# Optimization experiments

Measured on AMD Instinct MI355X. Metric: run time of the kernel, lower is better.

The kernel has to match this reference:

```python
import jax, jax.numpy as jnp
import numpy as np

DIM = 512
HEADS = 16
GRID = (32, 32)
MLP_HIDDEN = 2048
EPS = 1e-5


def _relative_position_index(hw):
    H, W = hw
    coords = np.stack(np.meshgrid(np.arange(H), np.arange(W), indexing='ij'))  # [2,H,W]
    coords = coords.reshape(2, -1)  # [2, L]
    rel = coords[:, :, None] - coords[:, None, :]  # [2, L, L]
    rel = rel.transpose(1, 2, 0).astype(np.int64)  # [L, L, 2]
    rel[:, :, 0] += H - 1
    rel[:, :, 1] += W - 1
    rel[:, :, 0] *= 2 * W - 1
    return jnp.asarray(rel.sum(-1))  # [L, L]


def setup_inputs() -> dict:
    key = jax.random.key(0)
    ks = jax.random.split(key, 12)
    L = GRID[0] * GRID[1]
    table_size = (2 * GRID[0] - 1) * (2 * GRID[1] - 1)
    s = 0.02
    return {
        'x': jax.random.normal(ks[0], (8, L, DIM), jnp.float32),
        'rel_index': _relative_position_index(GRID),
        'bias_table': s * jax.random.truncated_normal(ks[1], -2.0, 2.0, (table_size, HEADS), jnp.float32),
        'qkv_w': jax.random.normal(ks[2], (DIM, 3 * DIM), jnp.float32) / np.sqrt(DIM),
        'qkv_b': jnp.zeros((3 * DIM,), jnp.float32),
        'proj_w': jax.random.normal(ks[3], (DIM, DIM), jnp.float32) / np.sqrt(DIM),
        'proj_b': jnp.zeros((DIM,), jnp.float32),
        'n1_g': jnp.ones((DIM,), jnp.float32),
        'n1_b': jnp.zeros((DIM,), jnp.float32),
        'n2_g': jnp.ones((DIM,), jnp.float32),
        'n2_b': jnp.zeros((DIM,), jnp.float32),
        'fc1_w': jax.random.normal(ks[4], (DIM, MLP_HIDDEN), jnp.float32) / np.sqrt(DIM),
        'fc1_b': jnp.zeros((MLP_HIDDEN,), jnp.float32),
        'fc2_w': jax.random.normal(ks[5], (MLP_HIDDEN, DIM), jnp.float32) / np.sqrt(MLP_HIDDEN),
        'fc2_b': jnp.zeros((DIM,), jnp.float32),
    }


def _layernorm(x, g, b):
    mu = jnp.mean(x, -1, keepdims=True)
    var = jnp.mean(jnp.square(x - mu), -1, keepdims=True)
    return (x - mu) * jax.lax.rsqrt(var + EPS) * g + b


def reference(x, rel_index, bias_table, qkv_w, qkv_b, proj_w, proj_b,
              n1_g, n1_b, n2_g, n2_b, fc1_w, fc1_b, fc2_w, fc2_b):
    B, L, C = x.shape
    hd = C // HEADS
    scale = hd ** -0.5

    h = _layernorm(x, n1_g, n1_b)
    qkv = (h @ qkv_w + qkv_b).reshape(B, L, 3, HEADS, hd)
    qkv = jnp.transpose(qkv, (2, 0, 3, 1, 4))  # [3, B, H, L, hd]
    q, k, v = qkv[0] * scale, qkv[1], qkv[2]

    attn = jnp.einsum('bhld,bhmd->bhlm', q, k)  # [B, H, L, L]
    bias = bias_table[rel_index]                # [L, L, H]
    attn = attn + jnp.transpose(bias, (2, 0, 1))[None]
    attn = jax.nn.softmax(attn, axis=-1)

    out = jnp.einsum('bhlm,bhmd->bhld', attn, v)
    out = jnp.transpose(out, (0, 2, 1, 3)).reshape(B, L, C)
    out = out @ proj_w + proj_b

    x = x + out
    h2 = _layernorm(x, n2_g, n2_b)
    mlp = jax.nn.gelu(h2 @ fc1_w + fc1_b, approximate=False) @ fc2_w + fc2_b
    return x + mlp
```

## Files before the change

kernel.cpp:

```cpp
#include <hip/hip_runtime.h>

typedef unsigned short u16;
typedef __attribute__((ext_vector_type(8))) short bf16x8;
typedef __attribute__((ext_vector_type(4))) float f32x4;

__device__ __forceinline__ float bf2f(unsigned int u) {
    union { unsigned int i; float f; } c; c.i = u << 16; return c.f;
}
__device__ __forceinline__ unsigned int f2bf(float f) {
    union { float f; unsigned int i; } c; c.f = f;
    unsigned int x = c.i;
    unsigned int r = x + 0x7FFFu + ((x >> 16) & 1u);
    return r >> 16;
}

__device__ __forceinline__ void gload_lds16(const u16* g, u16* l) {
    __builtin_amdgcn_global_load_lds(
        (__attribute__((address_space(1))) void*)const_cast<u16*>(g),
        (__attribute__((address_space(3))) void*)l,
        16, 0, 0);
}

__global__ __launch_bounds__(256) void wconv_kernel(const float* __restrict__ W,
                                                    u16* __restrict__ Wt, int K, int N) {
    __shared__ u16 tile[32][36];
    int k0 = blockIdx.y * 32, n0 = blockIdx.x * 32;
    int t = threadIdx.x;
    int r = t >> 3, c4 = (t & 7) * 4;
    float4 v = *(const float4*)(W + (size_t)(k0 + r) * N + n0 + c4);
    tile[r][c4 + 0] = (u16)f2bf(v.x);
    tile[r][c4 + 1] = (u16)f2bf(v.y);
    tile[r][c4 + 2] = (u16)f2bf(v.z);
    tile[r][c4 + 3] = (u16)f2bf(v.w);
    __syncthreads();
    int n = t >> 3, k4 = (t & 7) * 4;
    u16 a0 = tile[k4 + 0][n], a1 = tile[k4 + 1][n];
    u16 a2 = tile[k4 + 2][n], a3 = tile[k4 + 3][n];
    uint2 st;
    st.x = (unsigned)a0 | ((unsigned)a1 << 16);
    st.y = (unsigned)a2 | ((unsigned)a3 << 16);
    *(uint2*)(Wt + (size_t)(n0 + n) * K + k0 + k4) = st;
}

__global__ __launch_bounds__(256) void ln_kernel(const float* __restrict__ x,
                                                 const float* __restrict__ g,
                                                 const float* __restrict__ b,
                                                 u16* __restrict__ y) {
    int row = blockIdx.x * 4 + (threadIdx.x >> 6);
    int t = threadIdx.x & 63;
    const float* xr = x + (size_t)row * 512 + t * 8;
    float4 a = *(const float4*)xr;
    float4 c = *(const float4*)(xr + 4);
    float v[8] = { a.x, a.y, a.z, a.w, c.x, c.y, c.z, c.w };
    float s = 0.f, ss = 0.f;
#pragma unroll
    for (int i = 0; i < 8; ++i) { s += v[i]; ss += v[i] * v[i]; }
#pragma unroll
    for (int off = 32; off; off >>= 1) {
        s  += __shfl_down(s, off);
        ss += __shfl_down(ss, off);
    }
    s = __shfl(s, 0); ss = __shfl(ss, 0);
    float mu = s * (1.0f / 512.0f);
    float var = ss * (1.0f / 512.0f) - mu * mu;
    float r = rsqrtf(var + 1e-5f);
    float4 g0 = *(const float4*)(g + t * 8);
    float4 g1 = *(const float4*)(g + t * 8 + 4);
    float4 b0 = *(const float4*)(b + t * 8);
    float4 b1 = *(const float4*)(b + t * 8 + 4);
    float gv[8] = { g0.x, g0.y, g0.z, g0.w, g1.x, g1.y, g1.z, g1.w };
    float bv[8] = { b0.x, b0.y, b0.z, b0.w, b1.x, b1.y, b1.z, b1.w };
    unsigned int o[4];
#pragma unroll
    for (int i = 0; i < 4; ++i) {
        float o0 = (v[2 * i] - mu) * r * gv[2 * i] + bv[2 * i];
        float o1 = (v[2 * i + 1] - mu) * r * gv[2 * i + 1] + bv[2 * i + 1];
        o[i] = f2bf(o0) | (f2bf(o1) << 16);
    }
    *(uint4*)(y + (size_t)row * 512 + t * 8) = make_uint4(o[0], o[1], o[2], o[3]);
}

template <int ACT, int RES, int COUT>
__global__ __launch_bounds__(256) void gemm_mfma(const u16* __restrict__ A, int lda,
                                                 const u16* __restrict__ Bt,
                                                 const float* __restrict__ bias,
                                                 const float* __restrict__ res, int ldres,
                                                 void* __restrict__ C, int ldC, int K) {
    __shared__ u16 As[128 * 32];
    __shared__ u16 Bs[128 * 32];
    int tid = threadIdx.x;
    int bm = blockIdx.y * 128, bn = blockIdx.x * 128;
    int lane = tid & 63, wv = tid >> 6;
    int q = lane >> 4, lr = lane & 15;
    int wr = wv >> 1, wc = wv & 1;

    const u16* Ag = A + (size_t)(bm + wv * 32 + (lane >> 2)) * lda + (lane & 3) * 8;
    const u16* Bg = Bt + (size_t)(bn + wv * 32 + (lane >> 2)) * K + (lane & 3) * 8;
    u16* Al0 = &As[(wv * 32) * 32];
    u16* Al1 = &As[(wv * 32 + 16) * 32];
    u16* Bl0 = &Bs[(wv * 32) * 32];
    u16* Bl1 = &Bs[(wv * 32 + 16) * 32];

    const u16* Apf = &As[(wr * 64 + lr) * 32 + q * 8];
    const u16* Bpf = &Bs[(wc * 64 + lr) * 32 + q * 8];

    f32x4 acc[4][4];
#pragma unroll
    for (int i = 0; i < 4; ++i)
#pragma unroll
        for (int j = 0; j < 4; ++j) acc[i][j] = (f32x4){0.f, 0.f, 0.f, 0.f};

    for (int k0 = 0; k0 < K; k0 += 32) {
        __syncthreads();
        gload_lds16(Ag + k0, Al0);
        gload_lds16(Ag + (size_t)16 * lda + k0, Al1);
        gload_lds16(Bg + k0, Bl0);
        gload_lds16(Bg + (size_t)16 * K + k0, Bl1);
        __syncthreads();
        bf16x8 af[4], bfr[4];
#pragma unroll
        for (int i = 0; i < 4; ++i) af[i] = *(const bf16x8*)(Apf + i * 16 * 32);
#pragma unroll
        for (int j = 0; j < 4; ++j) bfr[j] = *(const bf16x8*)(Bpf + j * 16 * 32);
#pragma unroll
        for (int i = 0; i < 4; ++i)
#pragma unroll
            for (int j = 0; j < 4; ++j)
                acc[i][j] = __builtin_amdgcn_mfma_f32_16x16x32_bf16(af[i], bfr[j], acc[i][j], 0, 0, 0);
    }

    float bv[4];
#pragma unroll
    for (int j = 0; j < 4; ++j)
        bv[j] = bias ? bias[bn + wc * 64 + j * 16 + lr] : 0.f;
#pragma unroll
    for (int i = 0; i < 4; ++i) {
#pragma unroll
        for (int j = 0; j < 4; ++j) {
            int col = bn + wc * 64 + j * 16 + lr;
#pragma unroll
            for (int r = 0; r < 4; ++r) {
                int row = bm + wr * 64 + i * 16 + q * 4 + r;
                float v = acc[i][j][r] + bv[j];
                if (ACT) v = 0.5f * v * (1.0f + erff(v * 0.7071067811865475f));
                if (RES) v += res[(size_t)row * ldres + col];
                if (COUT == 0) ((u16*)C)[(size_t)row * ldC + col] = (u16)f2bf(v);
                else           ((float*)C)[(size_t)row * ldC + col] = v;
            }
        }
    }
}

__global__ __launch_bounds__(256) void attn_mfma(u16* __restrict__ qkv,
                                                 const float* __restrict__ bias_table) {
    __shared__ u16 Ks[128][40];
    __shared__ u16 Vt[32][136];
    __shared__ u16 Ps[4][16][136];
    __shared__ float biasc[3969];
    int tid = threadIdx.x;
    int qt = blockIdx.x, h = blockIdx.y, z = blockIdx.z;
    u16* qkvz = qkv + (size_t)z * 1024 * 1536;

    for (int i = tid; i < 3969; i += 256) biasc[i] = bias_table[(size_t)i * 16 + h];

    int lane = tid & 63, wv = tid >> 6;
    int q = lane >> 4, m = lane & 15;

    int qrow = qt * 64 + wv * 16 + m;
    bf16x8 qf = *(const bf16x8*)(qkvz + (size_t)qrow * 1536 + h * 32 + q * 8);

    int arow[4];
#pragma unroll
    for (int r = 0; r < 4; ++r) {
        int l = qt * 64 + wv * 16 + q * 4 + r;
        arow[r] = (l >> 5) * 63 + (l & 31) + 1984;
    }

    const float scale = 0.17677669529663687f;
    float mrow[4] = { -1e30f, -1e30f, -1e30f, -1e30f };
    float lrow[4] = { 0.f, 0.f, 0.f, 0.f };
    f32x4 acco[2] = { (f32x4){0.f,0.f,0.f,0.f}, (f32x4){0.f,0.f,0.f,0.f} };

    int key = tid >> 1, dh = (tid & 1) * 16;
    const u16* kvsrc = qkvz + (size_t)key * 1536 + 512 + h * 32 + dh;
    uint4 pk0, pk1, pv0, pv1;
    pk0 = *(const uint4*)(kvsrc);
    pk1 = *(const uint4*)(kvsrc + 8);
    pv0 = *(const uint4*)(kvsrc + 512);
    pv1 = *(const uint4*)(kvsrc + 520);

    for (int kt = 0; kt < 8; ++kt) {
        __syncthreads();
        *(uint4*)&Ks[key][dh] = pk0;
        *(uint4*)&Ks[key][dh + 8] = pk1;
        {
            u16 tmp[16];
            *(uint4*)tmp = pv0; *(uint4*)(tmp + 8) = pv1;
#pragma unroll
            for (int j = 0; j < 16; ++j) Vt[dh + j][key] = tmp[j];
        }
        __syncthreads();
        if (kt < 7) {
            const u16* src = kvsrc + (size_t)(kt + 1) * 128 * 1536;
            pk0 = *(const uint4*)(src);
            pk1 = *(const uint4*)(src + 8);
            pv0 = *(const uint4*)(src + 512);
            pv1 = *(const uint4*)(src + 520);
        }

        f32x4 s8[8];
#pragma unroll
        for (int t = 0; t < 8; ++t) {
            bf16x8 kf = *(const bf16x8*)&Ks[t * 16 + m][q * 8];
            s8[t] = __builtin_amdgcn_mfma_f32_16x16x32_bf16(
                qf, kf, (f32x4){0.f,0.f,0.f,0.f}, 0, 0, 0);
        }
#pragma unroll
        for (int t = 0; t < 8; ++t) {
            int bb = (kt * 4 + (t >> 1)) * 63 + (t & 1) * 16 + m;
#pragma unroll
            for (int r = 0; r < 4; ++r)
                s8[t][r] = s8[t][r] * scale + biasc[arow[r] - bb];
        }
        float alpha[4];
#pragma unroll
        for (int r = 0; r < 4; ++r) {
            float v = s8[0][r];
#pragma unroll
            for (int t = 1; t < 8; ++t) v = fmaxf(v, s8[t][r]);
            v = fmaxf(v, __shfl_xor(v, 1));
            v = fmaxf(v, __shfl_xor(v, 2));
            v = fmaxf(v, __shfl_xor(v, 4));
            v = fmaxf(v, __shfl_xor(v, 8));
            float mn = fmaxf(mrow[r], v);
            alpha[r] = __expf(mrow[r] - mn);
            mrow[r] = mn;
            float sum = 0.f;
#pragma unroll
            for (int t = 0; t < 8; ++t) {
                float p = __expf(s8[t][r] - mn);
                s8[t][r] = p;
                sum += p;
            }
            sum += __shfl_xor(sum, 1);
            sum += __shfl_xor(sum, 2);
            sum += __shfl_xor(sum, 4);
            sum += __shfl_xor(sum, 8);
            lrow[r] = lrow[r] * alpha[r] + sum;
        }
#pragma unroll
        for (int t = 0; t < 8; ++t)
#pragma unroll
            for (int r = 0; r < 4; ++r)
                Ps[wv][q * 4 + r][t * 16 + m] = (u16)f2bf(s8[t][r]);
#pragma unroll
        for (int dt = 0; dt < 2; ++dt)
#pragma unroll
            for (int r = 0; r < 4; ++r) acco[dt][r] *= alpha[r];
#pragma unroll
        for (int c = 0; c < 4; ++c) {
            bf16x8 pf = *(const bf16x8*)&Ps[wv][m][c * 32 + q * 8];
#pragma unroll
            for (int dt = 0; dt < 2; ++dt) {
                bf16x8 vf = *(const bf16x8*)&Vt[dt * 16 + m][c * 32 + q * 8];
                acco[dt] = __builtin_amdgcn_mfma_f32_16x16x32_bf16(pf, vf, acco[dt], 0, 0, 0);
            }
        }
    }
#pragma unroll
    for (int r = 0; r < 4; ++r) {
        int l = qt * 64 + wv * 16 + q * 4 + r;
        float inv = 1.0f / lrow[r];
#pragma unroll
        for (int dt = 0; dt < 2; ++dt)
            qkvz[(size_t)l * 1536 + h * 32 + dt * 16 + m] = (u16)f2bf(acco[dt][r] * inv);
    }
}

extern "C" void kernel_launch(void* const* d_in, const int* in_sizes, int n_in,
                              void* d_out, int out_size, void* d_ws, size_t ws_size,
                              hipStream_t stream) {
    const float* x          = (const float*)d_in[0];
    const float* bias_table = (const float*)d_in[2];
    const float* qkv_w      = (const float*)d_in[3];
    const float* qkv_b      = (const float*)d_in[4];
    const float* proj_w     = (const float*)d_in[5];
    const float* proj_b     = (const float*)d_in[6];
    const float* n1g        = (const float*)d_in[7];
    const float* n1b        = (const float*)d_in[8];
    const float* n2g        = (const float*)d_in[9];
    const float* n2b        = (const float*)d_in[10];
    const float* fc1_w      = (const float*)d_in[11];
    const float* fc1_b      = (const float*)d_in[12];
    const float* fc2_w      = (const float*)d_in[13];
    const float* fc2_b      = (const float*)d_in[14];
    float* out = (float*)d_out;

    u16* ws16 = (u16*)d_ws;
    u16* wq_t = ws16;
    u16* wp_t = ws16 + 786432;
    u16* w1_t = ws16 + 1048576;
    u16* w2_t = ws16 + 2097152;
    u16* h    = ws16 + 3145728;
    u16* qkvb = ws16 + 7340032;
    u16* hid  = qkvb;

    wconv_kernel<<<dim3(48, 16), 256, 0, stream>>>(qkv_w, wq_t, 512, 1536);
    wconv_kernel<<<dim3(16, 16), 256, 0, stream>>>(proj_w, wp_t, 512, 512);
    wconv_kernel<<<dim3(64, 16), 256, 0, stream>>>(fc1_w, w1_t, 512, 2048);
    wconv_kernel<<<dim3(16, 64), 256, 0, stream>>>(fc2_w, w2_t, 2048, 512);

    ln_kernel<<<2048, 256, 0, stream>>>(x, n1g, n1b, h);

    for (int half = 0; half < 2; ++half) {
        size_t ro = (size_t)half * 4096;
        gemm_mfma<0, 0, 0><<<dim3(12, 32), 256, 0, stream>>>(
            h + ro * 512, 512, wq_t, qkv_b, nullptr, 0, qkvb, 1536, 512);
        attn_mfma<<<dim3(16, 16, 4), 256, 0, stream>>>(qkvb, bias_table);
        gemm_mfma<0, 1, 1><<<dim3(4, 32), 256, 0, stream>>>(
            qkvb, 1536, wp_t, proj_b, x + ro * 512, 512, out + ro * 512, 512, 512);
    }

    ln_kernel<<<2048, 256, 0, stream>>>(out, n2g, n2b, h);

    for (int half = 0; half < 2; ++half) {
        size_t ro = (size_t)half * 4096;
        gemm_mfma<1, 0, 0><<<dim3(16, 32), 256, 0, stream>>>(
            h + ro * 512, 512, w1_t, fc1_b, nullptr, 0, hid, 2048, 512);
        gemm_mfma<0, 1, 1><<<dim3(4, 32), 256, 0, stream>>>(
            hid, 2048, w2_t, fc2_b, out + ro * 512, 512, out + ro * 512, 512, 2048);
    }
}
```

Baseline: 425.2 us.

## Halve GEMM M-tile, fold softmax scale into Q with exp2, MFMA row sums

The GEMM block tile shrinks from 128x128 to 64x128 and the grids double, giving more blocks to fill the CUs at the cost of less reuse of B per block. In attention, the softmax scale and log2e are folded into Q and the bias cache so exp2f replaces __expf and the per-score multiply goes away. The softmax row sums and their shuffle reductions are replaced by an extra MFMA against a vector of ones, taking the sum from bf16-rounded probabilities. Rounding the scaled Q to bf16 adds a small precision change.

```diff
diff --git a/kernel.cpp b/kernel.cpp
--- a/kernel.cpp
+++ b/kernel.cpp
@@ -86,44 +86,42 @@
                                                  const float* __restrict__ bias,
                                                  const float* __restrict__ res, int ldres,
                                                  void* __restrict__ C, int ldC, int K) {
-    __shared__ u16 As[128 * 32];
+    __shared__ u16 As[64 * 32];
     __shared__ u16 Bs[128 * 32];
     int tid = threadIdx.x;
-    int bm = blockIdx.y * 128, bn = blockIdx.x * 128;
+    int bm = blockIdx.y * 64, bn = blockIdx.x * 128;
     int lane = tid & 63, wv = tid >> 6;
     int q = lane >> 4, lr = lane & 15;
     int wr = wv >> 1, wc = wv & 1;
 
-    const u16* Ag = A + (size_t)(bm + wv * 32 + (lane >> 2)) * lda + (lane & 3) * 8;
+    const u16* Ag = A + (size_t)(bm + wv * 16 + (lane >> 2)) * lda + (lane & 3) * 8;
     const u16* Bg = Bt + (size_t)(bn + wv * 32 + (lane >> 2)) * K + (lane & 3) * 8;
-    u16* Al0 = &As[(wv * 32) * 32];
-    u16* Al1 = &As[(wv * 32 + 16) * 32];
+    u16* Al0 = &As[(wv * 16) * 32];
     u16* Bl0 = &Bs[(wv * 32) * 32];
     u16* Bl1 = &Bs[(wv * 32 + 16) * 32];
 
-    const u16* Apf = &As[(wr * 64 + lr) * 32 + q * 8];
+    const u16* Apf = &As[(wr * 32 + lr) * 32 + q * 8];
     const u16* Bpf = &Bs[(wc * 64 + lr) * 32 + q * 8];
 
-    f32x4 acc[4][4];
-#pragma unroll
-    for (int i = 0; i < 4; ++i)
+    f32x4 acc[2][4];
+#pragma unroll
+    for (int i = 0; i < 2; ++i)
 #pragma unroll
         for (int j = 0; j < 4; ++j) acc[i][j] = (f32x4){0.f, 0.f, 0.f, 0.f};
 
     for (int k0 = 0; k0 < K; k0 += 32) {
         __syncthreads();
         gload_lds16(Ag + k0, Al0);
-        gload_lds16(Ag + (size_t)16 * lda + k0, Al1);
         gload_lds16(Bg + k0, Bl0);
         gload_lds16(Bg + (size_t)16 * K + k0, Bl1);
         __syncthreads();
-        bf16x8 af[4], bfr[4];
-#pragma unroll
-        for (int i = 0; i < 4; ++i) af[i] = *(const bf16x8*)(Apf + i * 16 * 32);
+        bf16x8 af[2], bfr[4];
+#pragma unroll
+        for (int i = 0; i < 2; ++i) af[i] = *(const bf16x8*)(Apf + i * 16 * 32);
 #pragma unroll
         for (int j = 0; j < 4; ++j) bfr[j] = *(const bf16x8*)(Bpf + j * 16 * 32);
 #pragma unroll
-        for (int i = 0; i < 4; ++i)
+        for (int i = 0; i < 2; ++i)
 #pragma unroll
             for (int j = 0; j < 4; ++j)
                 acc[i][j] = __builtin_amdgcn_mfma_f32_16x16x32_bf16(af[i], bfr[j], acc[i][j], 0, 0, 0);
@@ -134,13 +132,13 @@
     for (int j = 0; j < 4; ++j)
         bv[j] = bias ? bias[bn + wc * 64 + j * 16 + lr] : 0.f;
 #pragma unroll
-    for (int i = 0; i < 4; ++i) {
+    for (int i = 0; i < 2; ++i) {
 #pragma unroll
         for (int j = 0; j < 4; ++j) {
             int col = bn + wc * 64 + j * 16 + lr;
 #pragma unroll
             for (int r = 0; r < 4; ++r) {
-                int row = bm + wr * 64 + i * 16 + q * 4 + r;
+                int row = bm + wr * 32 + i * 16 + q * 4 + r;
                 float v = acc[i][j][r] + bv[j];
                 if (ACT) v = 0.5f * v * (1.0f + erff(v * 0.7071067811865475f));
                 if (RES) v += res[(size_t)row * ldres + col];
@@ -161,13 +159,21 @@
     int qt = blockIdx.x, h = blockIdx.y, z = blockIdx.z;
     u16* qkvz = qkv + (size_t)z * 1024 * 1536;
 
-    for (int i = tid; i < 3969; i += 256) biasc[i] = bias_table[(size_t)i * 16 + h];
+    const float LOG2E = 1.4426950408889634f;
+    for (int i = tid; i < 3969; i += 256) biasc[i] = bias_table[(size_t)i * 16 + h] * LOG2E;
 
     int lane = tid & 63, wv = tid >> 6;
     int q = lane >> 4, m = lane & 15;
 
     int qrow = qt * 64 + wv * 16 + m;
-    bf16x8 qf = *(const bf16x8*)(qkvz + (size_t)qrow * 1536 + h * 32 + q * 8);
+    bf16x8 qf;
+    {
+        const float qs = 0.17677669529663687f * LOG2E;
+        bf16x8 qraw = *(const bf16x8*)(qkvz + (size_t)qrow * 1536 + h * 32 + q * 8);
+#pragma unroll
+        for (int j = 0; j < 8; ++j)
+            qf[j] = (short)f2bf(bf2f((unsigned short)qraw[j]) * qs);
+    }
 
     int arow[4];
 #pragma unroll
@@ -176,10 +182,12 @@
         arow[r] = (l >> 5) * 63 + (l & 31) + 1984;
     }
 
-    const float scale = 0.17677669529663687f;
     float mrow[4] = { -1e30f, -1e30f, -1e30f, -1e30f };
-    float lrow[4] = { 0.f, 0.f, 0.f, 0.f };
-    f32x4 acco[2] = { (f32x4){0.f,0.f,0.f,0.f}, (f32x4){0.f,0.f,0.f,0.f} };
+    f32x4 acco[3] = { (f32x4){0.f,0.f,0.f,0.f}, (f32x4){0.f,0.f,0.f,0.f},
+                      (f32x4){0.f,0.f,0.f,0.f} };
+    bf16x8 onesv;
+#pragma unroll
+    for (int j = 0; j < 8; ++j) onesv[j] = (short)0x3F80;
 
     int key = tid >> 1, dh = (tid & 1) * 16;
     const u16* kvsrc = qkvz + (size_t)key * 1536 + 512 + h * 32 + dh;
@@ -220,7 +228,7 @@
             int bb = (kt * 4 + (t >> 1)) * 63 + (t & 1) * 16 + m;
 #pragma unroll
             for (int r = 0; r < 4; ++r)
-                s8[t][r] = s8[t][r] * scale + biasc[arow[r] - bb];
+                s8[t][r] += biasc[arow[r] - bb];
         }
         float alpha[4];
 #pragma unroll
@@ -233,20 +241,11 @@
             v = fmaxf(v, __shfl_xor(v, 4));
             v = fmaxf(v, __shfl_xor(v, 8));
             float mn = fmaxf(mrow[r], v);
-            alpha[r] = __expf(mrow[r] - mn);
+            alpha[r] = exp2f(mrow[r] - mn);
             mrow[r] = mn;
-            float sum = 0.f;
-#pragma unroll
-            for (int t = 0; t < 8; ++t) {
-                float p = __expf(s8[t][r] - mn);
-                s8[t][r] = p;
-                sum += p;
-            }
-            sum += __shfl_xor(sum, 1);
-            sum += __shfl_xor(sum, 2);
-            sum += __shfl_xor(sum, 4);
-            sum += __shfl_xor(sum, 8);
-            lrow[r] = lrow[r] * alpha[r] + sum;
+#pragma unroll
+            for (int t = 0; t < 8; ++t)
+                s8[t][r] = exp2f(s8[t][r] - mn);
         }
 #pragma unroll
         for (int t = 0; t < 8; ++t)
@@ -254,7 +253,7 @@
             for (int r = 0; r < 4; ++r)
                 Ps[wv][q * 4 + r][t * 16 + m] = (u16)f2bf(s8[t][r]);
 #pragma unroll
-        for (int dt = 0; dt < 2; ++dt)
+        for (int dt = 0; dt < 3; ++dt)
 #pragma unroll
             for (int r = 0; r < 4; ++r) acco[dt][r] *= alpha[r];
 #pragma unroll
@@ -265,12 +264,13 @@
                 bf16x8 vf = *(const bf16x8*)&Vt[dt * 16 + m][c * 32 + q * 8];
                 acco[dt] = __builtin_amdgcn_mfma_f32_16x16x32_bf16(pf, vf, acco[dt], 0, 0, 0);
             }
+            acco[2] = __builtin_amdgcn_mfma_f32_16x16x32_bf16(pf, onesv, acco[2], 0, 0, 0);
         }
     }
 #pragma unroll
     for (int r = 0; r < 4; ++r) {
         int l = qt * 64 + wv * 16 + q * 4 + r;
-        float inv = 1.0f / lrow[r];
+        float inv = 1.0f / acco[2][r];
 #pragma unroll
         for (int dt = 0; dt < 2; ++dt)
             qkvz[(size_t)l * 1536 + h * 32 + dt * 16 + m] = (u16)f2bf(acco[dt][r] * inv);
@@ -314,10 +314,10 @@
 
     for (int half = 0; half < 2; ++half) {
         size_t ro = (size_t)half * 4096;
-        gemm_mfma<0, 0, 0><<<dim3(12, 32), 256, 0, stream>>>(
+        gemm_mfma<0, 0, 0><<<dim3(12, 64), 256, 0, stream>>>(
             h + ro * 512, 512, wq_t, qkv_b, nullptr, 0, qkvb, 1536, 512);
         attn_mfma<<<dim3(16, 16, 4), 256, 0, stream>>>(qkvb, bias_table);
-        gemm_mfma<0, 1, 1><<<dim3(4, 32), 256, 0, stream>>>(
+        gemm_mfma<0, 1, 1><<<dim3(4, 64), 256, 0, stream>>>(
             qkvb, 1536, wp_t, proj_b, x + ro * 512, 512, out + ro * 512, 512, 512);
     }
 
@@ -325,9 +325,9 @@
 
     for (int half = 0; half < 2; ++half) {
         size_t ro = (size_t)half * 4096;
-        gemm_mfma<1, 0, 0><<<dim3(16, 32), 256, 0, stream>>>(
+        gemm_mfma<1, 0, 0><<<dim3(16, 64), 256, 0, stream>>>(
             h + ro * 512, 512, w1_t, fc1_b, nullptr, 0, hid, 2048, 512);
-        gemm_mfma<0, 1, 1><<<dim3(4, 32), 256, 0, stream>>>(
+        gemm_mfma<0, 1, 1><<<dim3(4, 64), 256, 0, stream>>>(
             hid, 2048, w2_t, fc2_b, out + ro * 512, 512, out + ro * 512, 512, 2048);
     }
 }
```

Result: faster. 395.2 us (-7.1%).
